# Kernel optimization log

Hardware: AMD Instinct MI355X
Metric: run time of the kernel (lower is better)

## Reference

```python
import jax, jax.numpy as jnp
import numpy as np

N, E, D, L, POS_VOC = 50000, 800000, 128, 3, 1024
EPS = 1e-5  # torch LayerNorm default


def layer_norm(x, g, b):
    m = jnp.mean(x, axis=-1, keepdims=True)
    v = jnp.var(x, axis=-1, keepdims=True)
    return (x - m) * jax.lax.rsqrt(v + EPS) * g + b


def setup_inputs() -> dict:
    key = jax.random.key(0)
    ks = jax.random.split(key, 8)
    node_emb = jax.random.normal(ks[0], (N, D), jnp.float32)
    pos = jax.random.randint(ks[1], (N,), 0, POS_VOC, dtype=jnp.int32)
    edge = jax.random.randint(ks[2], (2, E), 0, N, dtype=jnp.int32)
    # pos_embedding: xavier-uniform rows 1:, padding_idx=0 row zeroed
    lim = np.sqrt(6.0 / (POS_VOC - 1 + D))
    pos_table = jax.random.uniform(ks[3], (POS_VOC, D), jnp.float32, -lim, lim)
    pos_table = pos_table.at[0].set(0.0)
    # SAGEConv per layer: lin_l (with bias) on aggregated neighbors, lin_r (no bias) on root
    Wl = jax.random.normal(ks[4], (L, D, D), jnp.float32) / np.sqrt(D)
    bl = jnp.zeros((L, D), jnp.float32)
    Wr = jax.random.normal(ks[5], (L, D, D), jnp.float32) / np.sqrt(D)
    emb_ln_g = jnp.ones((D,), jnp.float32)
    emb_ln_b = jnp.zeros((D,), jnp.float32)
    hid_ln_g = jnp.ones((L, D), jnp.float32)
    hid_ln_b = jnp.zeros((L, D), jnp.float32)
    return dict(node_emb=node_emb, pos=pos, edge=edge, pos_table=pos_table,
                Wl=Wl, bl=bl, Wr=Wr, emb_ln_g=emb_ln_g, emb_ln_b=emb_ln_b,
                hid_ln_g=hid_ln_g, hid_ln_b=hid_ln_b)


def reference(node_emb, pos, edge, pos_table, Wl, bl, Wr,
              emb_ln_g, emb_ln_b, hid_ln_g, hid_ln_b):
    # embedding: scaled node emb + position embedding, then LayerNorm (dropout p=0 -> identity)
    x = node_emb * np.float32(np.sqrt(D)) + pos_table[pos]        # [N, D]
    x = layer_norm(x, emb_ln_g, emb_ln_b)
    src, dst = edge[0], edge[1]
    for i in range(L):
        # SAGEConv(aggr='add'): scatter-add neighbor feats, transform, add root transform
        agg = jax.ops.segment_sum(x[src], dst, num_segments=N)    # [N, D]
        h = agg @ Wl[i] + bl[i] + x @ Wr[i]                       # [N, D]
        h = jax.nn.relu(h)
        x = layer_norm(h + x, hid_ln_g[i], hid_ln_b[i])           # residual + LN
    return x
```

## Files before the change

kernel.cpp:

```cpp
#include <hip/hip_runtime.h>

#define DDIM    128
#define NNODES  50000
#define NEDGES  800000
#define NLAYERS 3
#define LN_EPS  1e-5f
#define CAP     96
#define NSLICE  8
#define SLICESZ ((NNODES + NSLICE - 1) / NSLICE)
#define FILL_EPT 8
#define FILL_CHUNK (256 * FILL_EPT)
#define FILL_NCHUNK ((NEDGES + FILL_CHUNK - 1) / FILL_CHUNK)

#define FILLB  (FILL_NCHUNK * NSLICE)
#define PAIRB  (2 * FILLB)
#define WPACKB ((NLAYERS * 4096 + 255) / 256)

typedef short s16x8 __attribute__((ext_vector_type(8)));
typedef float f32x4 __attribute__((ext_vector_type(4)));
typedef unsigned int u32;

__device__ __forceinline__ unsigned short f2bf(float f) {
    union { float f; unsigned u; } c; c.f = f;
    unsigned r = c.u + 0x7fff + ((c.u >> 16) & 1);
    return (unsigned short)(r >> 16);
}
__device__ __forceinline__ float bf2f_u(unsigned short h) {
    union { unsigned u; float f; } c; c.u = (unsigned)h << 16;
    return c.f;
}
__device__ __forceinline__ float bflo(u32 v) { return __uint_as_float(v << 16); }
__device__ __forceinline__ float bfhi(u32 v) { return __uint_as_float(v & 0xffff0000u); }

__global__ __launch_bounds__(256) void prep_kernel(
    const int* __restrict__ edge,
    int* __restrict__ cursor, int* __restrict__ srcs,
    const float* __restrict__ Wl, const float* __restrict__ Wr,
    unsigned short* __restrict__ wpk,
    const float* __restrict__ node_emb, const int* __restrict__ pos,
    const float* __restrict__ pos_table,
    const float* __restrict__ eg, const float* __restrict__ eb,
    uint4* __restrict__ xh4)
{
    int t = threadIdx.x;
    int bid = blockIdx.x;

    if (bid < PAIRB && (bid & 1) == 0) {
        int fi = bid >> 1;
        int slice = fi & (NSLICE - 1);
        int chunk = fi >> 3;
        int lo = slice * SLICESZ;
        int hi = lo + SLICESZ;
        int base = chunk * FILL_CHUNK + t * FILL_EPT;
        if (base < NEDGES) {
            int4 d0 = *(const int4*)(edge + NEDGES + base);
            int4 d1 = *(const int4*)(edge + NEDGES + base + 4);
            int4 s0 = *(const int4*)(edge + base);
            int4 s1 = *(const int4*)(edge + base + 4);
            int dd[8] = {d0.x, d0.y, d0.z, d0.w, d1.x, d1.y, d1.z, d1.w};
            int ss[8] = {s0.x, s0.y, s0.z, s0.w, s1.x, s1.y, s1.z, s1.w};
            #pragma unroll
            for (int i = 0; i < 8; ++i) {
                int d = dd[i];
                if (d >= lo && d < hi) {
                    int slot = atomicAdd(&cursor[d], 1);
                    srcs[d * CAP + slot] = ss[i];
                }
            }
        }
        return;
    }

    if (bid >= PAIRB) {
        int idx = (bid - PAIRB) * 256 + t;
        if (idx >= NLAYERS * 4096) return;
        int l   = idx >> 12;
        int rem = idx & 4095;
        int kt = rem >> 9, ct = (rem >> 6) & 7, ln = rem & 63;
        int k0 = kt * 32 + ((ln >> 4) << 3);
        int c  = ct * 16 + (ln & 15);
        const float* src = (kt < 4)
            ? Wl + (size_t)l * DDIM * DDIM + (size_t)k0 * DDIM + c
            : Wr + (size_t)l * DDIM * DDIM + (size_t)(k0 - 128) * DDIM + c;
        s16x8 o;
        #pragma unroll
        for (int j = 0; j < 8; ++j) o[j] = (short)f2bf(src[j * DDIM]);
        *(s16x8*)(wpk + (size_t)idx * 8) = o;
        return;
    }

    int bi = bid >> 1;
    int wv = (bi * 256 + t) >> 6;
    int lane = t & 63;
    int h = lane >> 4;
    int L = lane & 15;
    int n = wv * 4 + h;
    if (n >= NNODES) return;

    const float scale = 11.313708498984761f;
    int p = pos[n];

    const float* nb = node_emb + (size_t)n * DDIM + L * 8;
    const float* pb = pos_table + (size_t)p * DDIM + L * 8;
    float4 ne0 = *(const float4*)(nb);
    float4 ne1 = *(const float4*)(nb + 4);
    float4 pt0 = *(const float4*)(pb);
    float4 pt1 = *(const float4*)(pb + 4);

    float v[8];
    v[0] = ne0.x * scale + pt0.x;  v[1] = ne0.y * scale + pt0.y;
    v[2] = ne0.z * scale + pt0.z;  v[3] = ne0.w * scale + pt0.w;
    v[4] = ne1.x * scale + pt1.x;  v[5] = ne1.y * scale + pt1.y;
    v[6] = ne1.z * scale + pt1.z;  v[7] = ne1.w * scale + pt1.w;

    float s = 0.f, s2 = 0.f;
    #pragma unroll
    for (int k = 0; k < 8; ++k) { s += v[k]; s2 += v[k] * v[k]; }
    #pragma unroll
    for (int m = 8; m > 0; m >>= 1) {
        s  += __shfl_xor(s,  m, 64);
        s2 += __shfl_xor(s2, m, 64);
    }
    float mean = s * (1.0f / DDIM);
    float var  = s2 * (1.0f / DDIM) - mean * mean;
    float rstd = rsqrtf(var + LN_EPS);

    float4 gv0 = *(const float4*)(eg + L * 8);
    float4 gv1 = *(const float4*)(eg + L * 8 + 4);
    float4 bv0 = *(const float4*)(eb + L * 8);
    float4 bv1 = *(const float4*)(eb + L * 8 + 4);
    float gq[8] = {gv0.x, gv0.y, gv0.z, gv0.w, gv1.x, gv1.y, gv1.z, gv1.w};
    float bq[8] = {bv0.x, bv0.y, bv0.z, bv0.w, bv1.x, bv1.y, bv1.z, bv1.w};

    float y[8];
    #pragma unroll
    for (int k = 0; k < 8; ++k) y[k] = (v[k] - mean) * rstd * gq[k] + bq[k];

    uint4 o;
    o.x = (u32)f2bf(y[0]) | ((u32)f2bf(y[1]) << 16);
    o.y = (u32)f2bf(y[2]) | ((u32)f2bf(y[3]) << 16);
    o.z = (u32)f2bf(y[4]) | ((u32)f2bf(y[5]) << 16);
    o.w = (u32)f2bf(y[6]) | ((u32)f2bf(y[7]) << 16);
    xh4[(size_t)n * 16 + L] = o;
}

__global__ __launch_bounds__(256, 4) void sage_fused_kernel(
    const int* __restrict__ deg,
    const int* __restrict__ srcs,
    const uint4* __restrict__ xin4,
    const unsigned short* __restrict__ xin,
    const unsigned short* __restrict__ wpk,
    const float* __restrict__ bl,
    const float* __restrict__ g,
    const float* __restrict__ b,
    unsigned short* __restrict__ xh_out,
    float* __restrict__ xout)
{
    __shared__ unsigned short wlds[8192];
    __shared__ uint4 aggl[64 * 16];

    int t    = threadIdx.x;
    int wave = t >> 6;
    int lane = t & 63;
    int cl   = lane & 15;
    int q    = lane >> 4;

    {
        const s16x8* srcv = (const s16x8*)wpk;
        s16x8* dstv = (s16x8*)wlds;
        #pragma unroll
        for (int i = 0; i < 4; ++i) dstv[t + i * 256] = srcv[t + i * 256];
    }

    int m0 = blockIdx.x * 64;

    for (int r = 0; r < 4; ++r) {
        int nl = wave * 16 + r * 4 + q;
        int n  = m0 + nl;
        float acc[8];
        #pragma unroll
        for (int k = 0; k < 8; ++k) acc[k] = 0.f;
        if (n < NNODES) {
            int dg  = deg[n];
            int beg = n * CAP;
            for (int j = 0; j < dg; j += 8) {
                int sidx[8];
                #pragma unroll
                for (int c = 0; c < 8; ++c) {
                    int jj = j + c;
                    sidx[c] = (jj < dg) ? srcs[beg + jj] : -1;
                }
                uint4 u[8];
                #pragma unroll
                for (int c = 0; c < 8; ++c) {
                    u[c] = make_uint4(0u, 0u, 0u, 0u);
                    if (sidx[c] >= 0) u[c] = xin4[(size_t)sidx[c] * 16 + cl];
                }
                #pragma unroll
                for (int c = 0; c < 8; ++c) {
                    acc[0] += bflo(u[c].x); acc[1] += bfhi(u[c].x);
                    acc[2] += bflo(u[c].y); acc[3] += bfhi(u[c].y);
                    acc[4] += bflo(u[c].z); acc[5] += bfhi(u[c].z);
                    acc[6] += bflo(u[c].w); acc[7] += bfhi(u[c].w);
                }
            }
        }
        uint4 o;
        o.x = (u32)f2bf(acc[0]) | ((u32)f2bf(acc[1]) << 16);
        o.y = (u32)f2bf(acc[2]) | ((u32)f2bf(acc[3]) << 16);
        o.z = (u32)f2bf(acc[4]) | ((u32)f2bf(acc[5]) << 16);
        o.w = (u32)f2bf(acc[6]) | ((u32)f2bf(acc[7]) << 16);
        aggl[nl * 16 + (cl ^ (nl & 7))] = o;
    }

    int wbase = m0 + wave * 16;
    int mrow  = wave * 16 + cl;
    int m  = wbase + cl;
    int mc = (m < NNODES) ? m : (NNODES - 1);

    s16x8 af47[4];
    #pragma unroll
    for (int kt = 4; kt < 8; ++kt)
        af47[kt - 4] = *(const s16x8*)(xin + (size_t)mc * DDIM + (kt - 4) * 32 + q * 8);

    __syncthreads();

    f32x4 accm[8];
    #pragma unroll
    for (int ct = 0; ct < 8; ++ct) accm[ct] = (f32x4){0.f, 0.f, 0.f, 0.f};

    #pragma unroll
    for (int p = 0; p < 4; ++p) {
        #pragma unroll
        for (int kk = 0; kk < 2; ++kk) {
            int kt = p * 2 + kk;
            s16x8 af;
            if (kt < 4)
                af = *(const s16x8*)&aggl[mrow * 16 + ((kt * 4 + q) ^ (cl & 7))];
            else
                af = af47[kt - 4];
            #pragma unroll
            for (int ct = 0; ct < 8; ++ct) {
                s16x8 bfr = *(const s16x8*)&wlds[((((kk << 3) + ct) << 6) + lane) * 8];
                accm[ct] = __builtin_amdgcn_mfma_f32_16x16x32_bf16(af, bfr, accm[ct], 0, 0, 0);
            }
        }
        __syncthreads();
        if (p < 3) {
            const s16x8* srcv = (const s16x8*)(wpk + (size_t)(p + 1) * 8192);
            s16x8* dstv = (s16x8*)wlds;
            #pragma unroll
            for (int i = 0; i < 4; ++i) dstv[t + i * 256] = srcv[t + i * 256];
            __syncthreads();
        }
    }

    float bias[8], gg[8], bb[8];
    #pragma unroll
    for (int ct = 0; ct < 8; ++ct) {
        int c = ct * 16 + cl;
        bias[ct] = bl[c]; gg[ct] = g[c]; bb[ct] = b[c];
    }

    float hbuf[8][4];
    #pragma unroll
    for (int ct = 0; ct < 8; ++ct) {
        #pragma unroll
        for (int rr = 0; rr < 4; ++rr) {
            int node = wbase + q * 4 + rr;
            int nc   = (node < NNODES) ? node : (NNODES - 1);
            float hv = fmaxf(accm[ct][rr] + bias[ct], 0.0f);
            hbuf[ct][rr] = hv + bf2f_u(xin[(size_t)nc * DDIM + ct * 16 + cl]);
        }
    }

    float s[4], s2[4];
    #pragma unroll
    for (int rr = 0; rr < 4; ++rr) {
        float a0 = 0.f, a1 = 0.f;
        #pragma unroll
        for (int ct = 0; ct < 8; ++ct) {
            a0 += hbuf[ct][rr];
            a1 += hbuf[ct][rr] * hbuf[ct][rr];
        }
        #pragma unroll
        for (int msk = 1; msk < 16; msk <<= 1) {
            a0 += __shfl_xor(a0, msk, 64);
            a1 += __shfl_xor(a1, msk, 64);
        }
        s[rr] = a0; s2[rr] = a1;
    }

    #pragma unroll
    for (int rr = 0; rr < 4; ++rr) {
        int node = wbase + q * 4 + rr;
        if (node >= NNODES) continue;
        float mean = s[rr] * (1.0f / DDIM);
        float var  = s2[rr] * (1.0f / DDIM) - mean * mean;
        float rstd = rsqrtf(var + LN_EPS);
        #pragma unroll
        for (int ct = 0; ct < 8; ++ct) {
            float y = (hbuf[ct][rr] - mean) * rstd * gg[ct] + bb[ct];
            size_t off = (size_t)node * DDIM + ct * 16 + cl;
            if (xout) xout[off]    = y;
            else      xh_out[off]  = f2bf(y);
        }
    }
}

extern "C" void kernel_launch(void* const* d_in, const int* in_sizes, int n_in,
                              void* d_out, int out_size, void* d_ws, size_t ws_size,
                              hipStream_t stream)
{
    const float* node_emb = (const float*)d_in[0];
    const int*   pos      = (const int*)d_in[1];
    const int*   edge     = (const int*)d_in[2];
    const float* pos_tab  = (const float*)d_in[3];
    const float* Wl       = (const float*)d_in[4];
    const float* bl       = (const float*)d_in[5];
    const float* Wr       = (const float*)d_in[6];
    const float* eg       = (const float*)d_in[7];
    const float* eb       = (const float*)d_in[8];
    const float* hg       = (const float*)d_in[9];
    const float* hb       = (const float*)d_in[10];

    unsigned short* xA  = (unsigned short*)d_ws;
    unsigned short* xB  = xA + (size_t)NNODES * DDIM;
    unsigned short* wpk = xB + (size_t)NNODES * DDIM;
    int* cursor = (int*)(wpk + (size_t)NLAYERS * 4096 * 8);
    int* srcs   = cursor + NNODES;

    hipMemsetAsync(cursor, 0, NNODES * sizeof(int), stream);
    prep_kernel<<<PAIRB + WPACKB, 256, 0, stream>>>(
        edge, cursor, srcs, Wl, Wr, wpk,
        node_emb, pos, pos_tab, eg, eb, (uint4*)xA);

    for (int l = 0; l < NLAYERS; ++l) {
        unsigned short* xin = (l & 1) ? xB : xA;
        unsigned short* xo  = (l & 1) ? xA : xB;
        sage_fused_kernel<<<(NNODES + 63) / 64, 256, 0, stream>>>(
            cursor, srcs, (const uint4*)xin, xin,
            wpk + (size_t)l * 4096 * 8,
            bl + (size_t)l * DDIM,
            hg + (size_t)l * DDIM,
            hb + (size_t)l * DDIM,
            xo, (l == NLAYERS - 1) ? (float*)d_out : (float*)nullptr);
    }
}
```

Baseline: 245.8 us.

## Fuse prep and all SAGE layers into one persistent kernel with grid barriers

Measured after the change: 757.4 us. 208% more time.

```diff
diff --git a/kernel.cpp b/kernel.cpp
--- a/kernel.cpp
+++ b/kernel.cpp
@@ -15,6 +15,9 @@
 #define FILLB  (FILL_NCHUNK * NSLICE)
 #define PAIRB  (2 * FILLB)
 #define WPACKB ((NLAYERS * 4096 + 255) / 256)
+#define PREPU  (PAIRB + WPACKB)
+#define LAYERU ((NNODES + 63) / 64)
+#define MGRID  1024
 
 typedef short s16x8 __attribute__((ext_vector_type(8)));
 typedef float f32x4 __attribute__((ext_vector_type(4)));
@@ -32,147 +35,40 @@
 __device__ __forceinline__ float bflo(u32 v) { return __uint_as_float(v << 16); }
 __device__ __forceinline__ float bfhi(u32 v) { return __uint_as_float(v & 0xffff0000u); }
 
-__global__ __launch_bounds__(256) void prep_kernel(
-    const int* __restrict__ edge,
-    int* __restrict__ cursor, int* __restrict__ srcs,
-    const float* __restrict__ Wl, const float* __restrict__ Wr,
-    unsigned short* __restrict__ wpk,
-    const float* __restrict__ node_emb, const int* __restrict__ pos,
-    const float* __restrict__ pos_table,
-    const float* __restrict__ eg, const float* __restrict__ eb,
-    uint4* __restrict__ xh4)
+__device__ __forceinline__ void gbar(int* bar, int gen) {
+    __syncthreads();
+    if (threadIdx.x == 0) {
+        __threadfence();
+        atomicAdd(bar, 1);
+        while (atomicAdd(bar, 0) < gen * MGRID)
+            __builtin_amdgcn_s_sleep(32);
+    }
+    __syncthreads();
+    __threadfence();
+}
+
+__device__ __forceinline__ void layer_unit(
+    int u, int t,
+    const int* __restrict__ deg, const int* __restrict__ srcs,
+    const unsigned short* xin, const unsigned short* wl,
+    const float* bll, const float* gl, const float* bbl,
+    unsigned short* xo, float* xoutl,
+    unsigned short* wlds, uint4* aggl)
 {
-    int t = threadIdx.x;
-    int bid = blockIdx.x;
-
-    if (bid < PAIRB && (bid & 1) == 0) {
-        int fi = bid >> 1;
-        int slice = fi & (NSLICE - 1);
-        int chunk = fi >> 3;
-        int lo = slice * SLICESZ;
-        int hi = lo + SLICESZ;
-        int base = chunk * FILL_CHUNK + t * FILL_EPT;
-        if (base < NEDGES) {
-            int4 d0 = *(const int4*)(edge + NEDGES + base);
-            int4 d1 = *(const int4*)(edge + NEDGES + base + 4);
-            int4 s0 = *(const int4*)(edge + base);
-            int4 s1 = *(const int4*)(edge + base + 4);
-            int dd[8] = {d0.x, d0.y, d0.z, d0.w, d1.x, d1.y, d1.z, d1.w};
-            int ss[8] = {s0.x, s0.y, s0.z, s0.w, s1.x, s1.y, s1.z, s1.w};
-            #pragma unroll
-            for (int i = 0; i < 8; ++i) {
-                int d = dd[i];
-                if (d >= lo && d < hi) {
-                    int slot = atomicAdd(&cursor[d], 1);
-                    srcs[d * CAP + slot] = ss[i];
-                }
-            }
-        }
-        return;
-    }
-
-    if (bid >= PAIRB) {
-        int idx = (bid - PAIRB) * 256 + t;
-        if (idx >= NLAYERS * 4096) return;
-        int l   = idx >> 12;
-        int rem = idx & 4095;
-        int kt = rem >> 9, ct = (rem >> 6) & 7, ln = rem & 63;
-        int k0 = kt * 32 + ((ln >> 4) << 3);
-        int c  = ct * 16 + (ln & 15);
-        const float* src = (kt < 4)
-            ? Wl + (size_t)l * DDIM * DDIM + (size_t)k0 * DDIM + c
-            : Wr + (size_t)l * DDIM * DDIM + (size_t)(k0 - 128) * DDIM + c;
-        s16x8 o;
-        #pragma unroll
-        for (int j = 0; j < 8; ++j) o[j] = (short)f2bf(src[j * DDIM]);
-        *(s16x8*)(wpk + (size_t)idx * 8) = o;
-        return;
-    }
-
-    int bi = bid >> 1;
-    int wv = (bi * 256 + t) >> 6;
-    int lane = t & 63;
-    int h = lane >> 4;
-    int L = lane & 15;
-    int n = wv * 4 + h;
-    if (n >= NNODES) return;
-
-    const float scale = 11.313708498984761f;
-    int p = pos[n];
-
-    const float* nb = node_emb + (size_t)n * DDIM + L * 8;
-    const float* pb = pos_table + (size_t)p * DDIM + L * 8;
-    float4 ne0 = *(const float4*)(nb);
-    float4 ne1 = *(const float4*)(nb + 4);
-    float4 pt0 = *(const float4*)(pb);
-    float4 pt1 = *(const float4*)(pb + 4);
-
-    float v[8];
-    v[0] = ne0.x * scale + pt0.x;  v[1] = ne0.y * scale + pt0.y;
-    v[2] = ne0.z * scale + pt0.z;  v[3] = ne0.w * scale + pt0.w;
-    v[4] = ne1.x * scale + pt1.x;  v[5] = ne1.y * scale + pt1.y;
-    v[6] = ne1.z * scale + pt1.z;  v[7] = ne1.w * scale + pt1.w;
-
-    float s = 0.f, s2 = 0.f;
-    #pragma unroll
-    for (int k = 0; k < 8; ++k) { s += v[k]; s2 += v[k] * v[k]; }
-    #pragma unroll
-    for (int m = 8; m > 0; m >>= 1) {
-        s  += __shfl_xor(s,  m, 64);
-        s2 += __shfl_xor(s2, m, 64);
-    }
-    float mean = s * (1.0f / DDIM);
-    float var  = s2 * (1.0f / DDIM) - mean * mean;
-    float rstd = rsqrtf(var + LN_EPS);
-
-    float4 gv0 = *(const float4*)(eg + L * 8);
-    float4 gv1 = *(const float4*)(eg + L * 8 + 4);
-    float4 bv0 = *(const float4*)(eb + L * 8);
-    float4 bv1 = *(const float4*)(eb + L * 8 + 4);
-    float gq[8] = {gv0.x, gv0.y, gv0.z, gv0.w, gv1.x, gv1.y, gv1.z, gv1.w};
-    float bq[8] = {bv0.x, bv0.y, bv0.z, bv0.w, bv1.x, bv1.y, bv1.z, bv1.w};
-
-    float y[8];
-    #pragma unroll
-    for (int k = 0; k < 8; ++k) y[k] = (v[k] - mean) * rstd * gq[k] + bq[k];
-
-    uint4 o;
-    o.x = (u32)f2bf(y[0]) | ((u32)f2bf(y[1]) << 16);
-    o.y = (u32)f2bf(y[2]) | ((u32)f2bf(y[3]) << 16);
-    o.z = (u32)f2bf(y[4]) | ((u32)f2bf(y[5]) << 16);
-    o.w = (u32)f2bf(y[6]) | ((u32)f2bf(y[7]) << 16);
-    xh4[(size_t)n * 16 + L] = o;
-}
-
-__global__ __launch_bounds__(256, 4) void sage_fused_kernel(
-    const int* __restrict__ deg,
-    const int* __restrict__ srcs,
-    const uint4* __restrict__ xin4,
-    const unsigned short* __restrict__ xin,
-    const unsigned short* __restrict__ wpk,
-    const float* __restrict__ bl,
-    const float* __restrict__ g,
-    const float* __restrict__ b,
-    unsigned short* __restrict__ xh_out,
-    float* __restrict__ xout)
-{
-    __shared__ unsigned short wlds[8192];
-    __shared__ uint4 aggl[64 * 16];
-
-    int t    = threadIdx.x;
+    const uint4* xin4 = (const uint4*)xin;
     int wave = t >> 6;
     int lane = t & 63;
     int cl   = lane & 15;
     int q    = lane >> 4;
 
     {
-        const s16x8* srcv = (const s16x8*)wpk;
+        const s16x8* srcv = (const s16x8*)wl;
         s16x8* dstv = (s16x8*)wlds;
         #pragma unroll
         for (int i = 0; i < 4; ++i) dstv[t + i * 256] = srcv[t + i * 256];
     }
 
-    int m0 = blockIdx.x * 64;
+    int m0 = u * 64;
 
     for (int r = 0; r < 4; ++r) {
         int nl = wave * 16 + r * 4 + q;
@@ -190,18 +86,18 @@
                     int jj = j + c;
                     sidx[c] = (jj < dg) ? srcs[beg + jj] : -1;
                 }
-                uint4 u[8];
+                uint4 uu[8];
                 #pragma unroll
                 for (int c = 0; c < 8; ++c) {
-                    u[c] = make_uint4(0u, 0u, 0u, 0u);
-                    if (sidx[c] >= 0) u[c] = xin4[(size_t)sidx[c] * 16 + cl];
+                    uu[c] = make_uint4(0u, 0u, 0u, 0u);
+                    if (sidx[c] >= 0) uu[c] = xin4[(size_t)sidx[c] * 16 + cl];
                 }
                 #pragma unroll
                 for (int c = 0; c < 8; ++c) {
-                    acc[0] += bflo(u[c].x); acc[1] += bfhi(u[c].x);
-                    acc[2] += bflo(u[c].y); acc[3] += bfhi(u[c].y);
-                    acc[4] += bflo(u[c].z); acc[5] += bfhi(u[c].z);
-                    acc[6] += bflo(u[c].w); acc[7] += bfhi(u[c].w);
+                    acc[0] += bflo(uu[c].x); acc[1] += bfhi(uu[c].x);
+                    acc[2] += bflo(uu[c].y); acc[3] += bfhi(uu[c].y);
+                    acc[4] += bflo(uu[c].z); acc[5] += bfhi(uu[c].z);
+                    acc[6] += bflo(uu[c].w); acc[7] += bfhi(uu[c].w);
                 }
             }
         }
@@ -247,7 +143,7 @@
         }
         __syncthreads();
         if (p < 3) {
-            const s16x8* srcv = (const s16x8*)(wpk + (size_t)(p + 1) * 8192);
+            const s16x8* srcv = (const s16x8*)(wl + (size_t)(p + 1) * 8192);
             s16x8* dstv = (s16x8*)wlds;
             #pragma unroll
             for (int i = 0; i < 4; ++i) dstv[t + i * 256] = srcv[t + i * 256];
@@ -259,7 +155,7 @@
     #pragma unroll
     for (int ct = 0; ct < 8; ++ct) {
         int c = ct * 16 + cl;
-        bias[ct] = bl[c]; gg[ct] = g[c]; bb[ct] = b[c];
+        bias[ct] = bll[c]; gg[ct] = gl[c]; bb[ct] = bbl[c];
     }
 
     float hbuf[8][4];
@@ -302,9 +198,143 @@
         for (int ct = 0; ct < 8; ++ct) {
             float y = (hbuf[ct][rr] - mean) * rstd * gg[ct] + bb[ct];
             size_t off = (size_t)node * DDIM + ct * 16 + cl;
-            if (xout) xout[off]    = y;
-            else      xh_out[off]  = f2bf(y);
-        }
+            if (xoutl) xoutl[off] = y;
+            else       xo[off]    = f2bf(y);
+        }
+    }
+}
+
+__global__ __launch_bounds__(256, 4) void mega_kernel(
+    const int* __restrict__ edge,
+    int* cursor, int* srcs, int* bar,
+    const float* __restrict__ Wl, const float* __restrict__ bl,
+    const float* __restrict__ Wr,
+    unsigned short* wpk,
+    const float* __restrict__ node_emb, const int* __restrict__ pos,
+    const float* __restrict__ pos_table,
+    const float* __restrict__ eg, const float* __restrict__ eb,
+    const float* __restrict__ hg, const float* __restrict__ hb,
+    unsigned short* xA, unsigned short* xB, float* dout)
+{
+    __shared__ unsigned short wlds[8192];
+    __shared__ uint4 aggl[64 * 16];
+
+    int t = threadIdx.x;
+    int bid = blockIdx.x;
+
+    for (int uu = bid; uu < PREPU; uu += MGRID) {
+        if (uu < PAIRB && (uu & 1) == 0) {
+            int fi = uu >> 1;
+            int slice = fi & (NSLICE - 1);
+            int chunk = fi >> 3;
+            int lo = slice * SLICESZ;
+            int hi = lo + SLICESZ;
+            int base = chunk * FILL_CHUNK + t * FILL_EPT;
+            if (base < NEDGES) {
+                int4 d0 = *(const int4*)(edge + NEDGES + base);
+                int4 d1 = *(const int4*)(edge + NEDGES + base + 4);
+                int4 s0 = *(const int4*)(edge + base);
+                int4 s1 = *(const int4*)(edge + base + 4);
+                int dd[8] = {d0.x, d0.y, d0.z, d0.w, d1.x, d1.y, d1.z, d1.w};
+                int ss[8] = {s0.x, s0.y, s0.z, s0.w, s1.x, s1.y, s1.z, s1.w};
+                #pragma unroll
+                for (int i = 0; i < 8; ++i) {
+                    int d = dd[i];
+                    if (d >= lo && d < hi) {
+                        int slot = atomicAdd(&cursor[d], 1);
+                        srcs[d * CAP + slot] = ss[i];
+                    }
+                }
+            }
+        } else if (uu >= PAIRB) {
+            int idx = (uu - PAIRB) * 256 + t;
+            if (idx < NLAYERS * 4096) {
+                int l   = idx >> 12;
+                int rem = idx & 4095;
+                int kt = rem >> 9, ct = (rem >> 6) & 7, ln = rem & 63;
+                int k0 = kt * 32 + ((ln >> 4) << 3);
+                int c  = ct * 16 + (ln & 15);
+                const float* src = (kt < 4)
+                    ? Wl + (size_t)l * DDIM * DDIM + (size_t)k0 * DDIM + c
+                    : Wr + (size_t)l * DDIM * DDIM + (size_t)(k0 - 128) * DDIM + c;
+                s16x8 o;
+                #pragma unroll
+                for (int j = 0; j < 8; ++j) o[j] = (short)f2bf(src[j * DDIM]);
+                *(s16x8*)(wpk + (size_t)idx * 8) = o;
+            }
+        } else {
+            int bi = uu >> 1;
+            int wv = (bi * 256 + t) >> 6;
+            int lane = t & 63;
+            int h = lane >> 4;
+            int L = lane & 15;
+            int n = wv * 4 + h;
+            if (n < NNODES) {
+                const float scale = 11.313708498984761f;
+                int p = pos[n];
+                const float* nb = node_emb + (size_t)n * DDIM + L * 8;
+                const float* pb = pos_table + (size_t)p * DDIM + L * 8;
+                float4 ne0 = *(const float4*)(nb);
+                float4 ne1 = *(const float4*)(nb + 4);
+                float4 pt0 = *(const float4*)(pb);
+                float4 pt1 = *(const float4*)(pb + 4);
+
+                float v[8];
+                v[0] = ne0.x * scale + pt0.x;  v[1] = ne0.y * scale + pt0.y;
+                v[2] = ne0.z * scale + pt0.z;  v[3] = ne0.w * scale + pt0.w;
+                v[4] = ne1.x * scale + pt1.x;  v[5] = ne1.y * scale + pt1.y;
+                v[6] = ne1.z * scale + pt1.z;  v[7] = ne1.w * scale + pt1.w;
+
+                float s = 0.f, s2 = 0.f;
+                #pragma unroll
+                for (int k = 0; k < 8; ++k) { s += v[k]; s2 += v[k] * v[k]; }
+                #pragma unroll
+                for (int mm = 8; mm > 0; mm >>= 1) {
+                    s  += __shfl_xor(s,  mm, 64);
+                    s2 += __shfl_xor(s2, mm, 64);
+                }
+                float mean = s * (1.0f / DDIM);
+                float var  = s2 * (1.0f / DDIM) - mean * mean;
+                float rstd = rsqrtf(var + LN_EPS);
+
+                float4 gv0 = *(const float4*)(eg + L * 8);
+                float4 gv1 = *(const float4*)(eg + L * 8 + 4);
+                float4 bv0 = *(const float4*)(eb + L * 8);
+                float4 bv1 = *(const float4*)(eb + L * 8 + 4);
+                float gq[8] = {gv0.x, gv0.y, gv0.z, gv0.w, gv1.x, gv1.y, gv1.z, gv1.w};
+                float bq[8] = {bv0.x, bv0.y, bv0.z, bv0.w, bv1.x, bv1.y, bv1.z, bv1.w};
+
+                float y[8];
+                #pragma unroll
+                for (int k = 0; k < 8; ++k) y[k] = (v[k] - mean) * rstd * gq[k] + bq[k];
+
+                uint4 o;
+                o.x = (u32)f2bf(y[0]) | ((u32)f2bf(y[1]) << 16);
+                o.y = (u32)f2bf(y[2]) | ((u32)f2bf(y[3]) << 16);
+                o.z = (u32)f2bf(y[4]) | ((u32)f2bf(y[5]) << 16);
+                o.w = (u32)f2bf(y[6]) | ((u32)f2bf(y[7]) << 16);
+                ((uint4*)xA)[(size_t)n * 16 + L] = o;
+            }
+        }
+    }
+
+    gbar(bar, 1);
+
+    #pragma unroll 1
+    for (int l = 0; l < NLAYERS; ++l) {
+        const unsigned short* xin = (l & 1) ? xB : xA;
+        unsigned short* xo        = (l & 1) ? xA : xB;
+        const unsigned short* wl  = wpk + (size_t)l * 4096 * 8;
+        const float* bll = bl + (size_t)l * DDIM;
+        const float* gl  = hg + (size_t)l * DDIM;
+        const float* bbl = hb + (size_t)l * DDIM;
+        float* xoutl = (l == NLAYERS - 1) ? dout : (float*)nullptr;
+
+        if (bid < LAYERU)
+            layer_unit(bid, t, cursor, srcs, xin, wl, bll, gl, bbl,
+                       xo, xoutl, wlds, aggl);
+
+        if (l < NLAYERS - 1) gbar(bar, 2 + l);
     }
 }
 
@@ -328,22 +358,13 @@
     unsigned short* xB  = xA + (size_t)NNODES * DDIM;
     unsigned short* wpk = xB + (size_t)NNODES * DDIM;
     int* cursor = (int*)(wpk + (size_t)NLAYERS * 4096 * 8);
-    int* srcs   = cursor + NNODES;
-
-    hipMemsetAsync(cursor, 0, NNODES * sizeof(int), stream);
-    prep_kernel<<<PAIRB + WPACKB, 256, 0, stream>>>(
-        edge, cursor, srcs, Wl, Wr, wpk,
-        node_emb, pos, pos_tab, eg, eb, (uint4*)xA);
-
-    for (int l = 0; l < NLAYERS; ++l) {
-        unsigned short* xin = (l & 1) ? xB : xA;
-        unsigned short* xo  = (l & 1) ? xA : xB;
-        sage_fused_kernel<<<(NNODES + 63) / 64, 256, 0, stream>>>(
-            cursor, srcs, (const uint4*)xin, xin,
-            wpk + (size_t)l * 4096 * 8,
-            bl + (size_t)l * DDIM,
-            hg + (size_t)l * DDIM,
-            hb + (size_t)l * DDIM,
-            xo, (l == NLAYERS - 1) ? (float*)d_out : (float*)nullptr);
-    }
-}
+    int* bar    = cursor + NNODES;
+    int* srcs   = cursor + NNODES + 256;
+
+    hipMemsetAsync(cursor, 0, (NNODES + 256) * sizeof(int), stream);
+    mega_kernel<<<MGRID, 256, 0, stream>>>(
+        edge, cursor, srcs, bar,
+        Wl, bl, Wr, wpk,
+        node_emb, pos, pos_tab, eg, eb, hg, hb,
+        xA, xB, (float*)d_out);
+}
```
